# Performance work log

Measured on AMD Instinct MI355X. Metric: run time of the kernel, lower is better.

## Reference

```python
import jax, jax.numpy as jnp
import numpy as np

EPS = 1e-5

def layer_norm(x, g, b):
    mu = jnp.mean(x, axis=-1, keepdims=True)
    var = jnp.mean(jnp.square(x - mu), axis=-1, keepdims=True)
    return (x - mu) * jax.lax.rsqrt(var + EPS) * g + b

def setup_inputs() -> dict:
    key = jax.random.key(0)
    ks = jax.random.split(key, 16)
    B, C, H, W = 32, 128, 56, 56
    D = 64
    s = lambda fan: 1.0 / np.sqrt(fan)
    inp = {
        "x": jax.random.normal(ks[0], (B, C, H, W), dtype=jnp.float32),
        "We": jax.random.uniform(ks[1], (C, D), jnp.float32, -s(C), s(C)),
        "be": jax.random.uniform(ks[2], (D,), jnp.float32, -s(C), s(C)),
        "g1": jnp.ones((D,), jnp.float32), "b1": jnp.zeros((D,), jnp.float32),
        "g2": jnp.ones((D,), jnp.float32), "b2": jnp.zeros((D,), jnp.float32),
        "Wqkv": jax.random.uniform(ks[3], (D, 3 * D), jnp.float32, -s(D), s(D)),
        "bqkv": jax.random.uniform(ks[4], (3 * D,), jnp.float32, -s(D), s(D)),
        "Wp": jax.random.uniform(ks[5], (D, D), jnp.float32, -s(D), s(D)),
        "bp": jax.random.uniform(ks[6], (D,), jnp.float32, -s(D), s(D)),
        "gm": jnp.ones((D,), jnp.float32), "bm": jnp.zeros((D,), jnp.float32),
        "W1": jax.random.uniform(ks[7], (D, D), jnp.float32, -s(D), s(D)),
        "bm1": jax.random.uniform(ks[8], (D,), jnp.float32, -s(D), s(D)),
        "W2": jax.random.uniform(ks[9], (D, D), jnp.float32, -s(D), s(D)),
        "bm2": jax.random.uniform(ks[10], (D,), jnp.float32, -s(D), s(D)),
    }
    return inp

def reference(x, We, be, g1, b1, g2, b2, Wqkv, bqkv, Wp, bp, gm, bm, W1, bm1, W2, bm2):
    B, C, H, W = x.shape
    D = We.shape[1]
    # [B, C, H, W] -> [B, N, C], N = H*W tokens
    t = x.reshape(B, C, H * W).transpose(0, 2, 1)
    t = t @ We + be                                  # embed: [B, N, D]
    t = layer_norm(t, g1, b1)
    t = layer_norm(t, g2, b2)                        # dropout is identity at eval
    qkv = t @ Wqkv + bqkv                            # [B, N, 3D]
    q, k, v = jnp.split(qkv, 3, axis=-1)
    attn = jnp.einsum('bnd,bmd->bnm', q, k) * 0.125  # [B, N, N]
    attn = jax.nn.softmax(attn, axis=-1)
    t = jnp.einsum('bnm,bmd->bnd', attn, v)          # [B, N, D]
    t = t @ Wp + bp                                  # proj (dropout identity)
    h = layer_norm(t, gm, bm)
    h = jax.nn.gelu(h @ W1 + bm1, approximate=False)
    h = h @ W2 + bm2                                 # [B, N, D]
    out = h.transpose(0, 2, 1).reshape(B, D, H, W)
    return jnp.mean(out, axis=1, keepdims=True)      # [B, 1, H, W]
```

## Files before the change

### kernel.cpp

```cpp
#include <hip/hip_runtime.h>
#include <math.h>

#define TB 256
#define NB 32
#define NC 128
#define NHW 3136
#define ND 64
#define NT 49

typedef _Float16 half8 __attribute__((ext_vector_type(8)));
typedef _Float16 half4 __attribute__((ext_vector_type(4)));
typedef __fp16 fp16x2 __attribute__((ext_vector_type(2)));
typedef float float4v __attribute__((ext_vector_type(4)));

__device__ __forceinline__ void pack4h(_Float16* dst, float v0, float v1, float v2, float v3){
    union { fp16x2 h[2]; uint2 u; } pk;
    pk.h[0] = __builtin_amdgcn_cvt_pkrtz(v0, v1);
    pk.h[1] = __builtin_amdgcn_cvt_pkrtz(v2, v3);
    *(uint2*)dst = pk.u;
}
__device__ __forceinline__ half4 pack4v(float v0, float v1, float v2, float v3){
    union { fp16x2 h[2]; half4 v; } pk;
    pk.h[0] = __builtin_amdgcn_cvt_pkrtz(v0, v1);
    pk.h[1] = __builtin_amdgcn_cvt_pkrtz(v2, v3);
    return pk.v;
}

__global__ __launch_bounds__(TB) void k_prep(
    const float* __restrict__ We, const float* __restrict__ Wqkv,
    const float* __restrict__ Wp, const float* __restrict__ W1,
    const float* __restrict__ W2, const float* __restrict__ bm2,
    _Float16* __restrict__ WeT, _Float16* __restrict__ WqkvT,
    _Float16* __restrict__ WpT, _Float16* __restrict__ W1T,
    float* __restrict__ w2bx)
{
    const int t = blockIdx.x * TB + threadIdx.x;
    for (int i = t; i < 8192;  i += 2048) WeT[i]   = (_Float16)We[(i & 127) * 64 + (i >> 7)];
    for (int i = t; i < 12288; i += 2048) WqkvT[i] = (_Float16)Wqkv[(i & 63) * 192 + (i >> 6)];
    for (int i = t; i < 4096;  i += 2048) WpT[i]   = (_Float16)Wp[(i & 63) * 64 + (i >> 6)];
    for (int i = t; i < 4096;  i += 2048) W1T[i]   = (_Float16)W1[(i & 63) * 64 + (i >> 6)];
    if (t < 64) {
        float s = 0.f;
        for (int d = 0; d < 64; ++d) s += W2[t * 64 + d];
        w2bx[t] = s * (1.f / 64.f);
    }
    if (t == 64) {
        float s = 0.f;
        for (int d = 0; d < 64; ++d) s += bm2[d];
        w2bx[64] = s * (1.f / 64.f);
    }
}

__global__ __launch_bounds__(TB) void k_embed_qkv(
    const float* __restrict__ x,
    const float* __restrict__ be,
    const float* __restrict__ g1, const float* __restrict__ b1,
    const float* __restrict__ g2, const float* __restrict__ b2,
    const float* __restrict__ bqkv,
    const _Float16* __restrict__ WeT,
    const _Float16* __restrict__ WqkvT,
    _Float16* __restrict__ qh, _Float16* __restrict__ khb, _Float16* __restrict__ vtb)
{
    __shared__ float xs[128 * 66];
    __shared__ _Float16 zL[4 * 16 * 72];
    __shared__ _Float16 vt16[64 * 72];

    const int b = blockIdx.y, n0 = blockIdx.x * 64, tid = threadIdx.x;
    const int w = tid >> 6, lane = tid & 63, quad = lane >> 4, cl = lane & 15;

    {
        const int cb = tid >> 4, tok4 = (tid & 15) * 4;
        const float* xb = x + (size_t)b * NC * NHW + n0 + tok4;
        #pragma unroll
        for (int p = 0; p < 8; ++p) {
            const int c = p * 16 + cb;
            float4 v = *(const float4*)(xb + (size_t)c * NHW);
            float* dst = &xs[c * 66 + tok4];
            *(float2*)dst = make_float2(v.x, v.y);
            *(float2*)(dst + 2) = make_float2(v.z, v.w);
        }
    }
    __syncthreads();

    half8 bx[4];
    #pragma unroll
    for (int ck = 0; ck < 4; ++ck) {
        const float* xp = &xs[(ck * 32 + quad * 8) * 66 + w * 16 + cl];
        union { fp16x2 h[4]; half8 v; } u;
        #pragma unroll
        for (int jj = 0; jj < 4; ++jj)
            u.h[jj] = __builtin_amdgcn_cvt_pkrtz(xp[(2 * jj) * 66], xp[(2 * jj + 1) * 66]);
        bx[ck] = u.v;
    }

    float tv[4][4];
    #pragma unroll
    for (int dt = 0; dt < 4; ++dt) {
        float4v acc = (float4v){0.f, 0.f, 0.f, 0.f};
        #pragma unroll
        for (int ck = 0; ck < 4; ++ck) {
            half8 af = *(const half8*)(WeT + (dt * 16 + cl) * 128 + ck * 32 + quad * 8);
            acc = __builtin_amdgcn_mfma_f32_16x16x32_f16(af, bx[ck], acc, 0, 0, 0);
        }
        float4 bev = *(const float4*)(be + dt * 16 + quad * 4);
        const float* bevp = (const float*)&bev;
        #pragma unroll
        for (int r = 0; r < 4; ++r) tv[dt][r] = acc[r] + bevp[r];
    }

    #pragma unroll
    for (int ln = 0; ln < 2; ++ln) {
        float sm = 0.f;
        #pragma unroll
        for (int dt = 0; dt < 4; ++dt)
            #pragma unroll
            for (int r = 0; r < 4; ++r) sm += tv[dt][r];
        sm += __shfl_xor(sm, 16); sm += __shfl_xor(sm, 32);
        const float mu = sm * (1.f / 64.f);
        float vr = 0.f;
        #pragma unroll
        for (int dt = 0; dt < 4; ++dt)
            #pragma unroll
            for (int r = 0; r < 4; ++r) { float d = tv[dt][r] - mu; vr += d * d; }
        vr += __shfl_xor(vr, 16); vr += __shfl_xor(vr, 32);
        const float is = rsqrtf(vr * (1.f / 64.f) + 1e-5f);
        const float* gp = (ln == 0) ? g1 : g2;
        const float* bp_ = (ln == 0) ? b1 : b2;
        #pragma unroll
        for (int dt = 0; dt < 4; ++dt) {
            float4 gq = *(const float4*)(gp + dt * 16 + quad * 4);
            float4 bq = *(const float4*)(bp_ + dt * 16 + quad * 4);
            const float* gqp = (const float*)&gq;
            const float* bqp = (const float*)&bq;
            #pragma unroll
            for (int r = 0; r < 4; ++r)
                tv[dt][r] = (tv[dt][r] - mu) * is * gqp[r] + bqp[r];
        }
    }

    _Float16* zw = zL + w * (16 * 72);
    #pragma unroll
    for (int dt = 0; dt < 4; ++dt)
        *(half4*)&zw[cl * 72 + dt * 16 + quad * 4] = pack4v(tv[dt][0], tv[dt][1], tv[dt][2], tv[dt][3]);
    __asm__ __volatile__("s_waitcnt lgkmcnt(0)" ::: "memory");
    half8 bz[2];
    #pragma unroll
    for (int ck = 0; ck < 2; ++ck)
        bz[ck] = *(const half8*)&zw[cl * 72 + ck * 32 + quad * 8];

    const float QSC = 0.125f * 1.44269504088896f;
    const int tok = w * 16 + cl;
    #pragma unroll
    for (int et = 0; et < 12; ++et) {
        float4v acc = (float4v){0.f, 0.f, 0.f, 0.f};
        #pragma unroll
        for (int ck = 0; ck < 2; ++ck) {
            half8 af = *(const half8*)(WqkvT + (et * 16 + cl) * 64 + ck * 32 + quad * 8);
            acc = __builtin_amdgcn_mfma_f32_16x16x32_f16(af, bz[ck], acc, 0, 0, 0);
        }
        float4 bq = *(const float4*)(bqkv + et * 16 + quad * 4);
        const float* bqp = (const float*)&bq;
        float vv[4];
        #pragma unroll
        for (int r = 0; r < 4; ++r) vv[r] = acc[r] + bqp[r];
        if (et < 4) {
            pack4h(qh + ((size_t)(b * NHW + n0 + tok)) * ND + et * 16 + quad * 4,
                   vv[0] * QSC, vv[1] * QSC, vv[2] * QSC, vv[3] * QSC);
        } else if (et < 8) {
            pack4h(khb + ((size_t)(b * NHW + n0 + tok)) * ND + (et - 4) * 16 + quad * 4,
                   vv[0], vv[1], vv[2], vv[3]);
        } else {
            #pragma unroll
            for (int r = 0; r < 4; ++r)
                vt16[((et - 8) * 16 + quad * 4 + r) * 72 + tok] = (_Float16)vv[r];
        }
    }
    __syncthreads();
    #pragma unroll
    for (int i = 0; i < 2; ++i) {
        int ch = tid + 256 * i;
        int row = ch >> 3, off = (ch & 7) * 8;
        *(uint4*)(vtb + ((size_t)(b * ND + row)) * NHW + n0 + off) =
            *(const uint4*)&vt16[row * 72 + off];
    }
}

__global__ __launch_bounds__(TB) void k_attn(
    const _Float16* __restrict__ qh, const _Float16* __restrict__ khb,
    const _Float16* __restrict__ vtb, _Float16* __restrict__ ob)
{
    __shared__ _Float16 Kb[2][64 * 72];
    __shared__ _Float16 Vb[2][64 * 72];

    const int b    = blockIdx.y;
    const int n0   = blockIdx.x * 128;
    const int tid  = threadIdx.x;
    const int w    = tid >> 6;
    const int lane = tid & 63;
    const int quad = lane >> 4;
    const int c    = lane & 15;
    const float CEXP = 4.0f * 1.44269504088896f;

    half8 qf[2][2];
    #pragma unroll
    for (int qt = 0; qt < 2; ++qt) {
        int row = n0 + w * 32 + qt * 16 + c;
        row = row < NHW ? row : NHW - 1;
        const _Float16* qp = qh + ((size_t)(b * NHW + row)) * ND + quad * 8;
        qf[qt][0] = *(const half8*)(qp);
        qf[qt][1] = *(const half8*)(qp + 32);
    }

    float4v o[2][4];
    #pragma unroll
    for (int qt = 0; qt < 2; ++qt)
        #pragma unroll
        for (int nt = 0; nt < 4; ++nt) o[qt][nt] = (float4v){0.f, 0.f, 0.f, 0.f};
    float lp[2] = {0.f, 0.f};

    const _Float16* kbase = khb + ((size_t)b * NHW) * ND;
    const _Float16* vbase = vtb + ((size_t)b * ND) * NHW;

    const int row0 = (tid + 0)   >> 3, off0 = ((tid + 0)   & 7) * 8;
    const int row1 = (tid + 256) >> 3, off1 = ((tid + 256) & 7) * 8;

    uint4 pk0, pk1, pv0, pv1;
    pk0 = *(const uint4*)(kbase + (size_t)row0 * ND + off0);
    pk1 = *(const uint4*)(kbase + (size_t)row1 * ND + off1);
    pv0 = *(const uint4*)(vbase + (size_t)row0 * NHW + off0);
    pv1 = *(const uint4*)(vbase + (size_t)row1 * NHW + off1);

    for (int kt = 0; kt < NT; ++kt) {
        const int bsel = kt & 1;
        __syncthreads();
        *(uint4*)&Kb[bsel][row0 * 72 + off0] = pk0;
        *(uint4*)&Kb[bsel][row1 * 72 + off1] = pk1;
        *(uint4*)&Vb[bsel][row0 * 72 + off0] = pv0;
        *(uint4*)&Vb[bsel][row1 * 72 + off1] = pv1;
        if (kt + 1 < NT) {
            const _Float16* kp = kbase + (size_t)((kt + 1) * 64) * ND;
            const _Float16* vp = vbase + (kt + 1) * 64;
            pk0 = *(const uint4*)(kp + (size_t)row0 * ND + off0);
            pk1 = *(const uint4*)(kp + (size_t)row1 * ND + off1);
            pv0 = *(const uint4*)(vp + (size_t)row0 * NHW + off0);
            pv1 = *(const uint4*)(vp + (size_t)row1 * NHW + off1);
        }
        __syncthreads();

        half8 ka[4][2];
        #pragma unroll
        for (int mt = 0; mt < 4; ++mt) {
            const _Float16* kp = &Kb[bsel][(mt * 16 + c) * 72 + quad * 8];
            ka[mt][0] = *(const half8*)(kp);
            ka[mt][1] = *(const half8*)(kp + 32);
        }

        float4v s[2][4];
        #pragma unroll
        for (int qt = 0; qt < 2; ++qt)
            #pragma unroll
            for (int mt = 0; mt < 4; ++mt) {
                float4v z = (float4v){0.f, 0.f, 0.f, 0.f};
                z = __builtin_amdgcn_mfma_f32_16x16x32_f16(ka[mt][0], qf[qt][0], z, 0, 0, 0);
                z = __builtin_amdgcn_mfma_f32_16x16x32_f16(ka[mt][1], qf[qt][1], z, 0, 0, 0);
                s[qt][mt] = z;
            }

        half4 pb[2][4];
        #pragma unroll
        for (int qt = 0; qt < 2; ++qt) {
            float ls = 0.f;
            #pragma unroll
            for (int mt = 0; mt < 4; ++mt) {
                #pragma unroll
                for (int r = 0; r < 4; ++r) {
                    float p = __builtin_amdgcn_exp2f(s[qt][mt][r] - CEXP);
                    s[qt][mt][r] = p;
                    ls += p;
                }
                pb[qt][mt] = pack4v(s[qt][mt][0], s[qt][mt][1], s[qt][mt][2], s[qt][mt][3]);
            }
            lp[qt] += ls;
        }

        #pragma unroll
        for (int nt = 0; nt < 4; ++nt) {
            #pragma unroll
            for (int mt = 0; mt < 4; ++mt) {
                half4 vv = *(const half4*)&Vb[bsel][(nt * 16 + c) * 72 + mt * 16 + quad * 4];
                #pragma unroll
                for (int qt = 0; qt < 2; ++qt)
                    o[qt][nt] = __builtin_amdgcn_mfma_f32_16x16x16f16(vv, pb[qt][mt], o[qt][nt], 0, 0, 0);
            }
        }
    }

    #pragma unroll
    for (int qt = 0; qt < 2; ++qt) {
        float lq = lp[qt];
        lq += __shfl_xor(lq, 16); lq += __shfl_xor(lq, 32);
        float inv = 1.f / lq;
        int row = n0 + w * 32 + qt * 16 + c;
        if (row < NHW) {
            _Float16* op = ob + ((size_t)(b * NHW + row)) * ND + quad * 4;
            #pragma unroll
            for (int nt = 0; nt < 4; ++nt)
                pack4h(op + nt * 16, o[qt][nt][0] * inv, o[qt][nt][1] * inv,
                       o[qt][nt][2] * inv, o[qt][nt][3] * inv);
        }
    }
}

__global__ __launch_bounds__(TB) void k_post(
    const _Float16* __restrict__ aih,
    const float* __restrict__ bp,
    const float* __restrict__ gm, const float* __restrict__ bm,
    const float* __restrict__ bm1,
    const _Float16* __restrict__ WpT, const _Float16* __restrict__ W1T,
    const float* __restrict__ w2bx,
    float* __restrict__ out)
{
    __shared__ _Float16 zL2[4 * 16 * 72];

    const int b = blockIdx.y, n0 = blockIdx.x * 64, tid = threadIdx.x;
    const int w = tid >> 6, lane = tid & 63, quad = lane >> 4, cl = lane & 15;
    const int tok = w * 16 + cl;

    const _Float16* ap = aih + ((size_t)(b * NHW + n0 + tok)) * ND;
    half8 ba[2];
    ba[0] = *(const half8*)(ap + quad * 8);
    ba[1] = *(const half8*)(ap + 32 + quad * 8);

    float uv[4][4];
    #pragma unroll
    for (int et = 0; et < 4; ++et) {
        float4v acc = (float4v){0.f, 0.f, 0.f, 0.f};
        #pragma unroll
        for (int ck = 0; ck < 2; ++ck) {
            half8 af = *(const half8*)(WpT + (et * 16 + cl) * 64 + ck * 32 + quad * 8);
            acc = __builtin_amdgcn_mfma_f32_16x16x32_f16(af, ba[ck], acc, 0, 0, 0);
        }
        float4 bq = *(const float4*)(bp + et * 16 + quad * 4);
        const float* bqp = (const float*)&bq;
        #pragma unroll
        for (int r = 0; r < 4; ++r) uv[et][r] = acc[r] + bqp[r];
    }

    {
        float sm = 0.f;
        #pragma unroll
        for (int et = 0; et < 4; ++et)
            #pragma unroll
            for (int r = 0; r < 4; ++r) sm += uv[et][r];
        sm += __shfl_xor(sm, 16); sm += __shfl_xor(sm, 32);
        const float mu = sm * (1.f / 64.f);
        float vr = 0.f;
        #pragma unroll
        for (int et = 0; et < 4; ++et)
            #pragma unroll
            for (int r = 0; r < 4; ++r) { float d = uv[et][r] - mu; vr += d * d; }
        vr += __shfl_xor(vr, 16); vr += __shfl_xor(vr, 32);
        const float is = rsqrtf(vr * (1.f / 64.f) + 1e-5f);
        #pragma unroll
        for (int et = 0; et < 4; ++et) {
            float4 gq = *(const float4*)(gm + et * 16 + quad * 4);
            float4 bq = *(const float4*)(bm + et * 16 + quad * 4);
            const float* gqp = (const float*)&gq;
            const float* bqp = (const float*)&bq;
            #pragma unroll
            for (int r = 0; r < 4; ++r)
                uv[et][r] = (uv[et][r] - mu) * is * gqp[r] + bqp[r];
        }
    }

    _Float16* zw = zL2 + w * (16 * 72);
    #pragma unroll
    for (int et = 0; et < 4; ++et)
        *(half4*)&zw[cl * 72 + et * 16 + quad * 4] = pack4v(uv[et][0], uv[et][1], uv[et][2], uv[et][3]);
    __asm__ __volatile__("s_waitcnt lgkmcnt(0)" ::: "memory");
    half8 bz[2];
    #pragma unroll
    for (int ck = 0; ck < 2; ++ck)
        bz[ck] = *(const half8*)&zw[cl * 72 + ck * 32 + quad * 8];

    float part = 0.f;
    #pragma unroll
    for (int et = 0; et < 4; ++et) {
        float4v acc = (float4v){0.f, 0.f, 0.f, 0.f};
        #pragma unroll
        for (int ck = 0; ck < 2; ++ck) {
            half8 af = *(const half8*)(W1T + (et * 16 + cl) * 64 + ck * 32 + quad * 8);
            acc = __builtin_amdgcn_mfma_f32_16x16x32_f16(af, bz[ck], acc, 0, 0, 0);
        }
        float4 b1q = *(const float4*)(bm1 + et * 16 + quad * 4);
        float4 wq  = *(const float4*)(w2bx + et * 16 + quad * 4);
        const float* b1p = (const float*)&b1q;
        const float* wqp = (const float*)&wq;
        #pragma unroll
        for (int r = 0; r < 4; ++r) {
            float h = acc[r] + b1p[r];
            float g = 0.5f * h * (1.f + erff(h * 0.70710678118654752f));
            part = fmaf(g, wqp[r], part);
        }
    }
    part += __shfl_xor(part, 16); part += __shfl_xor(part, 32);
    if (lane < 16)
        out[(size_t)b * NHW + n0 + tok] = part + w2bx[64];
}

extern "C" void kernel_launch(void* const* d_in, const int* in_sizes, int n_in,
                              void* d_out, int out_size, void* d_ws, size_t ws_size,
                              hipStream_t stream) {
    (void)in_sizes; (void)n_in; (void)out_size; (void)ws_size;
    const float* x    = (const float*)d_in[0];
    const float* We   = (const float*)d_in[1];
    const float* be   = (const float*)d_in[2];
    const float* g1   = (const float*)d_in[3];
    const float* b1   = (const float*)d_in[4];
    const float* g2   = (const float*)d_in[5];
    const float* b2   = (const float*)d_in[6];
    const float* Wqkv = (const float*)d_in[7];
    const float* bqkv = (const float*)d_in[8];
    const float* Wp   = (const float*)d_in[9];
    const float* bp   = (const float*)d_in[10];
    const float* gm   = (const float*)d_in[11];
    const float* bm   = (const float*)d_in[12];
    const float* W1   = (const float*)d_in[13];
    const float* bm1  = (const float*)d_in[14];
    const float* W2   = (const float*)d_in[15];
    const float* bm2  = (const float*)d_in[16];
    float* out = (float*)d_out;

    const size_t NQ = (size_t)NB * NHW * ND;
    _Float16* qh    = (_Float16*)d_ws;
    _Float16* khb   = qh + NQ;
    _Float16* vtb   = khb + NQ;
    _Float16* obf   = vtb + NQ;
    _Float16* WeT   = obf + NQ;
    _Float16* WqkvT = WeT + 64 * 128;
    _Float16* WpT   = WqkvT + 192 * 64;
    _Float16* W1T   = WpT + 64 * 64;
    float*    w2bx  = (float*)(W1T + 64 * 64);

    dim3 blk(TB);
    k_prep<<<dim3(8), blk, 0, stream>>>(We, Wqkv, Wp, W1, W2, bm2, WeT, WqkvT, WpT, W1T, w2bx);
    k_embed_qkv<<<dim3(NT, NB), blk, 0, stream>>>(x, be, g1, b1, g2, b2, bqkv, WeT, WqkvT, qh, khb, vtb);
    k_attn<<<dim3(25, NB), blk, 0, stream>>>(qh, khb, vtb, obf);
    k_post<<<dim3(NT, NB), blk, 0, stream>>>(obf, bp, gm, bm, bm1, WpT, W1T, w2bx, out);
}
```

Before: 330.0 us.

## Drop redundant attention barrier, pad LDS strides, fold biases into MFMA accumulators

In the attention loop, the next tile is now stored to the alternate LDS buffer before a single barrier, and the second __syncthreads per iteration is removed. This relies on double buffering to keep the single barrier safe. The K and V LDS row strides change from 72 to 76 and 74 halves to alter bank mapping. Those strides are no longer multiples of the 16-byte and 8-byte vector access sizes, so the vector LDS accesses become misaligned. Biases and the softmax exp offset are preloaded into the MFMA accumulators instead of being added afterwards, and the attention grid is transposed so batch is the fast block index.

```diff
diff --git a/kernel.cpp b/kernel.cpp
--- a/kernel.cpp
+++ b/kernel.cpp
@@ -7,6 +7,8 @@
 #define NHW 3136
 #define ND 64
 #define NT 49
+#define KST 76
+#define VST 74
 
 typedef _Float16 half8 __attribute__((ext_vector_type(8)));
 typedef _Float16 half4 __attribute__((ext_vector_type(4)));
@@ -96,16 +98,15 @@
     float tv[4][4];
     #pragma unroll
     for (int dt = 0; dt < 4; ++dt) {
-        float4v acc = (float4v){0.f, 0.f, 0.f, 0.f};
+        float4 bev = *(const float4*)(be + dt * 16 + quad * 4);
+        float4v acc = (float4v){bev.x, bev.y, bev.z, bev.w};
         #pragma unroll
         for (int ck = 0; ck < 4; ++ck) {
             half8 af = *(const half8*)(WeT + (dt * 16 + cl) * 128 + ck * 32 + quad * 8);
             acc = __builtin_amdgcn_mfma_f32_16x16x32_f16(af, bx[ck], acc, 0, 0, 0);
         }
-        float4 bev = *(const float4*)(be + dt * 16 + quad * 4);
-        const float* bevp = (const float*)&bev;
-        #pragma unroll
-        for (int r = 0; r < 4; ++r) tv[dt][r] = acc[r] + bevp[r];
+        #pragma unroll
+        for (int r = 0; r < 4; ++r) tv[dt][r] = acc[r];
     }
 
     #pragma unroll
@@ -152,27 +153,23 @@
     const int tok = w * 16 + cl;
     #pragma unroll
     for (int et = 0; et < 12; ++et) {
-        float4v acc = (float4v){0.f, 0.f, 0.f, 0.f};
+        float4 bq = *(const float4*)(bqkv + et * 16 + quad * 4);
+        float4v acc = (float4v){bq.x, bq.y, bq.z, bq.w};
         #pragma unroll
         for (int ck = 0; ck < 2; ++ck) {
             half8 af = *(const half8*)(WqkvT + (et * 16 + cl) * 64 + ck * 32 + quad * 8);
             acc = __builtin_amdgcn_mfma_f32_16x16x32_f16(af, bz[ck], acc, 0, 0, 0);
         }
-        float4 bq = *(const float4*)(bqkv + et * 16 + quad * 4);
-        const float* bqp = (const float*)&bq;
-        float vv[4];
-        #pragma unroll
-        for (int r = 0; r < 4; ++r) vv[r] = acc[r] + bqp[r];
         if (et < 4) {
             pack4h(qh + ((size_t)(b * NHW + n0 + tok)) * ND + et * 16 + quad * 4,
-                   vv[0] * QSC, vv[1] * QSC, vv[2] * QSC, vv[3] * QSC);
+                   acc[0] * QSC, acc[1] * QSC, acc[2] * QSC, acc[3] * QSC);
         } else if (et < 8) {
             pack4h(khb + ((size_t)(b * NHW + n0 + tok)) * ND + (et - 4) * 16 + quad * 4,
-                   vv[0], vv[1], vv[2], vv[3]);
+                   acc[0], acc[1], acc[2], acc[3]);
         } else {
             #pragma unroll
             for (int r = 0; r < 4; ++r)
-                vt16[((et - 8) * 16 + quad * 4 + r) * 72 + tok] = (_Float16)vv[r];
+                vt16[((et - 8) * 16 + quad * 4 + r) * 72 + tok] = (_Float16)acc[r];
         }
     }
     __syncthreads();
@@ -189,11 +186,11 @@
     const _Float16* __restrict__ qh, const _Float16* __restrict__ khb,
     const _Float16* __restrict__ vtb, _Float16* __restrict__ ob)
 {
-    __shared__ _Float16 Kb[2][64 * 72];
-    __shared__ _Float16 Vb[2][64 * 72];
-
-    const int b    = blockIdx.y;
-    const int n0   = blockIdx.x * 128;
+    __shared__ _Float16 Kb[2][64 * KST];
+    __shared__ _Float16 Vb[2][64 * VST];
+
+    const int b    = blockIdx.x;
+    const int n0   = blockIdx.y * 128;
     const int tid  = threadIdx.x;
     const int w    = tid >> 6;
     const int lane = tid & 63;
@@ -232,11 +229,11 @@
 
     for (int kt = 0; kt < NT; ++kt) {
         const int bsel = kt & 1;
+        *(uint4*)&Kb[bsel][row0 * KST + off0] = pk0;
+        *(uint4*)&Kb[bsel][row1 * KST + off1] = pk1;
+        *(uint4*)&Vb[bsel][row0 * VST + off0] = pv0;
+        *(uint4*)&Vb[bsel][row1 * VST + off1] = pv1;
         __syncthreads();
-        *(uint4*)&Kb[bsel][row0 * 72 + off0] = pk0;
-        *(uint4*)&Kb[bsel][row1 * 72 + off1] = pk1;
-        *(uint4*)&Vb[bsel][row0 * 72 + off0] = pv0;
-        *(uint4*)&Vb[bsel][row1 * 72 + off1] = pv1;
         if (kt + 1 < NT) {
             const _Float16* kp = kbase + (size_t)((kt + 1) * 64) * ND;
             const _Float16* vp = vbase + (kt + 1) * 64;
@@ -245,12 +242,11 @@
             pv0 = *(const uint4*)(vp + (size_t)row0 * NHW + off0);
             pv1 = *(const uint4*)(vp + (size_t)row1 * NHW + off1);
         }
-        __syncthreads();
 
         half8 ka[4][2];
         #pragma unroll
         for (int mt = 0; mt < 4; ++mt) {
-            const _Float16* kp = &Kb[bsel][(mt * 16 + c) * 72 + quad * 8];
+            const _Float16* kp = &Kb[bsel][(mt * 16 + c) * KST + quad * 8];
             ka[mt][0] = *(const half8*)(kp);
             ka[mt][1] = *(const half8*)(kp + 32);
         }
@@ -260,7 +256,7 @@
         for (int qt = 0; qt < 2; ++qt)
             #pragma unroll
             for (int mt = 0; mt < 4; ++mt) {
-                float4v z = (float4v){0.f, 0.f, 0.f, 0.f};
+                float4v z = (float4v){-CEXP, -CEXP, -CEXP, -CEXP};
                 z = __builtin_amdgcn_mfma_f32_16x16x32_f16(ka[mt][0], qf[qt][0], z, 0, 0, 0);
                 z = __builtin_amdgcn_mfma_f32_16x16x32_f16(ka[mt][1], qf[qt][1], z, 0, 0, 0);
                 s[qt][mt] = z;
@@ -274,7 +270,7 @@
             for (int mt = 0; mt < 4; ++mt) {
                 #pragma unroll
                 for (int r = 0; r < 4; ++r) {
-                    float p = __builtin_amdgcn_exp2f(s[qt][mt][r] - CEXP);
+                    float p = __builtin_amdgcn_exp2f(s[qt][mt][r]);
                     s[qt][mt][r] = p;
                     ls += p;
                 }
@@ -287,7 +283,7 @@
         for (int nt = 0; nt < 4; ++nt) {
             #pragma unroll
             for (int mt = 0; mt < 4; ++mt) {
-                half4 vv = *(const half4*)&Vb[bsel][(nt * 16 + c) * 72 + mt * 16 + quad * 4];
+                half4 vv = *(const half4*)&Vb[bsel][(nt * 16 + c) * VST + mt * 16 + quad * 4];
                 #pragma unroll
                 for (int qt = 0; qt < 2; ++qt)
                     o[qt][nt] = __builtin_amdgcn_mfma_f32_16x16x16f16(vv, pb[qt][mt], o[qt][nt], 0, 0, 0);
@@ -334,16 +330,15 @@
     float uv[4][4];
     #pragma unroll
     for (int et = 0; et < 4; ++et) {
-        float4v acc = (float4v){0.f, 0.f, 0.f, 0.f};
+        float4 bq = *(const float4*)(bp + et * 16 + quad * 4);
+        float4v acc = (float4v){bq.x, bq.y, bq.z, bq.w};
         #pragma unroll
         for (int ck = 0; ck < 2; ++ck) {
             half8 af = *(const half8*)(WpT + (et * 16 + cl) * 64 + ck * 32 + quad * 8);
             acc = __builtin_amdgcn_mfma_f32_16x16x32_f16(af, ba[ck], acc, 0, 0, 0);
         }
-        float4 bq = *(const float4*)(bp + et * 16 + quad * 4);
-        const float* bqp = (const float*)&bq;
-        #pragma unroll
-        for (int r = 0; r < 4; ++r) uv[et][r] = acc[r] + bqp[r];
+        #pragma unroll
+        for (int r = 0; r < 4; ++r) uv[et][r] = acc[r];
     }
 
     {
@@ -386,19 +381,18 @@
     float part = 0.f;
     #pragma unroll
     for (int et = 0; et < 4; ++et) {
-        float4v acc = (float4v){0.f, 0.f, 0.f, 0.f};
+        float4 b1q = *(const float4*)(bm1 + et * 16 + quad * 4);
+        float4v acc = (float4v){b1q.x, b1q.y, b1q.z, b1q.w};
         #pragma unroll
         for (int ck = 0; ck < 2; ++ck) {
             half8 af = *(const half8*)(W1T + (et * 16 + cl) * 64 + ck * 32 + quad * 8);
             acc = __builtin_amdgcn_mfma_f32_16x16x32_f16(af, bz[ck], acc, 0, 0, 0);
         }
-        float4 b1q = *(const float4*)(bm1 + et * 16 + quad * 4);
-        float4 wq  = *(const float4*)(w2bx + et * 16 + quad * 4);
-        const float* b1p = (const float*)&b1q;
+        float4 wq = *(const float4*)(w2bx + et * 16 + quad * 4);
         const float* wqp = (const float*)&wq;
         #pragma unroll
         for (int r = 0; r < 4; ++r) {
-            float h = acc[r] + b1p[r];
+            float h = acc[r];
             float g = 0.5f * h * (1.f + erff(h * 0.70710678118654752f));
             part = fmaf(g, wqp[r], part);
         }
@@ -445,6 +439,6 @@
     dim3 blk(TB);
     k_prep<<<dim3(8), blk, 0, stream>>>(We, Wqkv, Wp, W1, W2, bm2, WeT, WqkvT, WpT, W1T, w2bx);
     k_embed_qkv<<<dim3(NT, NB), blk, 0, stream>>>(x, be, g1, b1, g2, b2, bqkv, WeT, WqkvT, qh, khb, vtb);
-    k_attn<<<dim3(25, NB), blk, 0, stream>>>(qh, khb, vtb, obf);
+    k_attn<<<dim3(NB, 25), blk, 0, stream>>>(qh, khb, vtb, obf);
     k_post<<<dim3(NT, NB), blk, 0, stream>>>(obf, bp, gm, bm, bm1, WpT, W1T, w2bx, out);
 }
```

After: 456.9 us. 1.38x slower.
